# Kernel tuning notes

Measured on AMD Instinct MI355X. Metric: run time of the kernel, lower is better.

The kernel has to match this reference:

```python
import jax, jax.numpy as jnp
import numpy as np

D_MODEL = 1024
NUM_HEADS = 16
HEAD_DIM = D_MODEL // NUM_HEADS
THETA = 10000.0


def setup_inputs() -> dict:
    key = jax.random.key(0)
    k1, k2, k3 = jax.random.split(key, 3)
    B, S = 4, 2048
    x = jax.random.normal(k1, (B, S, D_MODEL), dtype=jnp.float32)
    token_positions = jnp.arange(S, dtype=jnp.int32)
    std_qkv = 2.0 / (D_MODEL + 3 * D_MODEL)
    std_o = 2.0 / (D_MODEL + D_MODEL)
    W_qkv = jax.random.normal(k2, (3 * D_MODEL, D_MODEL), dtype=jnp.float32) * std_qkv
    W_o = jax.random.normal(k3, (D_MODEL, D_MODEL), dtype=jnp.float32) * std_o
    return {"x": x, "token_positions": token_positions, "W_qkv": W_qkv, "W_o": W_o}


def _apply_rope(x, positions):
    # x: [B, H, S, d]; positions: [S]
    d = x.shape[-1]
    inv_freq = 1.0 / THETA ** (2.0 * jnp.arange(0, d // 2, dtype=jnp.float32) / d)
    angle = positions.astype(jnp.float32)[:, None] * inv_freq[None, :]  # [S, d/2]
    cos, sin = jnp.cos(angle), jnp.sin(angle)
    x1, x2 = x[..., 0::2], x[..., 1::2]
    rot = jnp.stack([x1 * cos - x2 * sin, x2 * cos + x1 * sin], axis=-1)
    return rot.reshape(x.shape)


def reference(x, token_positions, W_qkv, W_o):
    B, S, D = x.shape
    H, hd = NUM_HEADS, HEAD_DIM
    qkv = jnp.einsum('bsi,ji->bsj', x, W_qkv)            # [B, S, 3D]
    qkv = qkv.reshape(B, S, 3, H, hd).transpose(2, 0, 3, 1, 4)  # [3, B, H, S, hd]
    q, k, v = qkv[0], qkv[1], qkv[2]
    q = _apply_rope(q, token_positions)
    k = _apply_rope(k, token_positions)
    scores = jnp.einsum('bhqd,bhkd->bhqk', q, k) / jnp.sqrt(jnp.float32(hd))
    causal = jnp.tril(jnp.ones((S, S), dtype=bool))
    scores = jnp.where(causal, scores, -jnp.inf)
    probs = jax.nn.softmax(scores, axis=-1)
    attn = jnp.einsum('bhqk,bhkd->bhqd', probs, v)       # [B, H, S, hd]
    attn = attn.transpose(0, 2, 1, 3).reshape(B, S, D)
    return jnp.einsum('bsi,ji->bsj', attn, W_o)
```

## Files before the change

kernel.cpp:

```cpp
#include <hip/hip_runtime.h>

#define B_ 4
#define S_ 2048
#define D_ 1024
#define H_ 16
#define HD_ 64
#define M_ (B_*S_)
#define NQKV_ (3*D_)

typedef _Float16 f16;
typedef __attribute__((ext_vector_type(4))) _Float16 f16x4;
typedef __attribute__((ext_vector_type(8))) _Float16 f16x8;
typedef __attribute__((ext_vector_type(4))) float f32x4;
typedef __attribute__((ext_vector_type(16))) float f32x16;

__device__ __forceinline__ void gload_lds16(const void* g, void* lds) {
  __builtin_amdgcn_global_load_lds(
      (const __attribute__((address_space(1))) void*)g,
      (__attribute__((address_space(3))) void*)lds, 16, 0, 0);
}

__global__ void cast_kernel(const float* __restrict__ in, f16* __restrict__ out) {
  size_t i = (size_t)(blockIdx.x * 256 + threadIdx.x) * 8;
  float4 a = *reinterpret_cast<const float4*>(in + i);
  float4 b = *reinterpret_cast<const float4*>(in + i + 4);
  f16x8 o;
  o[0] = (f16)a.x; o[1] = (f16)a.y; o[2] = (f16)a.z; o[3] = (f16)a.w;
  o[4] = (f16)b.x; o[5] = (f16)b.y; o[6] = (f16)b.z; o[7] = (f16)b.w;
  *reinterpret_cast<f16x8*>(out + i) = o;
}

__global__ void trig_kernel(const int* __restrict__ pos, float2* __restrict__ tab) {
  int idx = blockIdx.x * 256 + threadIdx.x;
  int s = idx >> 5, t = idx & 31;
  float p = (float)pos[s];
  float invf = exp2f((float)t * -0.4152410118609203f);
  float sn, cs;
  sincosf(p * invf, &sn, &cs);
  tab[idx] = float2{cs, sn};
}

template <int MODE>
__global__ __launch_bounds__(512)
void gemm_bt(const f16* __restrict__ A, const f16* __restrict__ Bt,
             void* __restrict__ Cout, const float2* __restrict__ tab,
             f16* __restrict__ kout, f16* __restrict__ vtout,
             int M, int N, int K) {
  __shared__ __align__(16) f16 As[3][128 * 64];
  __shared__ __align__(16) f16 Bs[3][256 * 64];
  const int tid = threadIdx.x;
  const int w = tid >> 6, l = tid & 63;
  const int nM = M >> 7;
  const int bm = (blockIdx.x % nM) << 7;
  const int bn = (blockIdx.x / nM) << 8;
  const int wrow = (w >> 2) << 6;
  const int wcol = (w & 3) << 6;
  const int lr = l & 15;
  const int lk = (l >> 4) << 3;
  const int orow = (l >> 4) << 2;
  const int swz = (lr & 7) << 3;

  f32x4 acc[4][4];
  #pragma unroll
  for (int i = 0; i < 4; ++i)
    #pragma unroll
    for (int j = 0; j < 4; ++j) acc[i][j] = f32x4{0.f, 0.f, 0.f, 0.f};

  const int sc8 = (tid & 7) * 8;
  const int NT = K >> 6;

  #define STAGE(t_) {                                                         \
    const int buf_ = (t_) % 3, k0_ = (t_) << 6;                               \
    _Pragma("unroll")                                                         \
    for (int i = 0; i < 2; ++i) {                                             \
      int row = (i * 512 + tid) >> 3;                                         \
      gload_lds16(A + (size_t)(bm + row) * K + k0_ + (sc8 ^ ((row & 7) << 3)),\
                  (void*)(&As[buf_][(i * 512 + tid) * 8]));                   \
    }                                                                         \
    _Pragma("unroll")                                                         \
    for (int i = 0; i < 4; ++i) {                                             \
      int row = (i * 512 + tid) >> 3;                                         \
      gload_lds16(Bt + (size_t)(bn + row) * K + k0_ + (sc8 ^ ((row & 7) << 3)),\
                  (void*)(&Bs[buf_][(i * 512 + tid) * 8]));                   \
    }                                                                         \
  }

  STAGE(0);
  STAGE(1);

  for (int t = 0; t < NT; ++t) {
    if (t < NT - 1) {
      asm volatile("s_waitcnt vmcnt(6)" ::: "memory");
    } else {
      asm volatile("s_waitcnt vmcnt(0)" ::: "memory");
    }
    __builtin_amdgcn_sched_barrier(0);
    __builtin_amdgcn_s_barrier();
    __builtin_amdgcn_sched_barrier(0);
    if (t + 2 < NT) STAGE(t + 2);

    const f16* Asc = As[t % 3];
    const f16* Bsc = Bs[t % 3];
    #pragma unroll
    for (int ts = 0; ts < 2; ++ts) {
      f16x8 af[4], bfr[4];
      #pragma unroll
      for (int mi = 0; mi < 4; ++mi)
        af[mi] = *reinterpret_cast<const f16x8*>(
            Asc + (wrow + mi * 16 + lr) * 64 + ((ts * 32 + lk) ^ swz));
      #pragma unroll
      for (int ni = 0; ni < 4; ++ni)
        bfr[ni] = *reinterpret_cast<const f16x8*>(
            Bsc + (wcol + ni * 16 + lr) * 64 + ((ts * 32 + lk) ^ swz));
      #pragma unroll
      for (int mi = 0; mi < 4; ++mi)
        #pragma unroll
        for (int ni = 0; ni < 4; ++ni)
          acc[mi][ni] = __builtin_amdgcn_mfma_f32_16x16x32_f16(bfr[ni], af[mi], acc[mi][ni], 0, 0, 0);
    }
  }
  #undef STAGE

  if (MODE == 0) {
    const int which = bn >> 10;
    const int h = ((bn + wcol) >> 6) & (H_ - 1);
    if (which < 2) {
      f16* dst = which ? kout : (f16*)Cout;
      const float qs = which ? 1.0f : 0.125f * 1.4426950408889634f;
      #pragma unroll
      for (int mi = 0; mi < 4; ++mi) {
        int m = bm + wrow + mi * 16 + lr;
        int b = m >> 11, s = m & (S_ - 1);
        size_t rowbase = ((size_t)(b * H_ + h) * S_ + s) * HD_;
        const float4* trow = reinterpret_cast<const float4*>(tab + (size_t)s * 32);
        #pragma unroll
        for (int ni = 0; ni < 4; ++ni) {
          int d0 = ni * 16 + orow;
          float4 cssn = trow[d0 >> 2];
          float x0 = acc[mi][ni][0], x1 = acc[mi][ni][1];
          float x2 = acc[mi][ni][2], x3 = acc[mi][ni][3];
          f16x4 ov;
          ov[0] = (f16)((x0 * cssn.x - x1 * cssn.y) * qs);
          ov[1] = (f16)((x1 * cssn.x + x0 * cssn.y) * qs);
          ov[2] = (f16)((x2 * cssn.z - x3 * cssn.w) * qs);
          ov[3] = (f16)((x3 * cssn.z + x2 * cssn.w) * qs);
          *reinterpret_cast<f16x4*>(&dst[rowbase + d0]) = ov;
        }
      }
    } else {
      #pragma unroll
      for (int mi = 0; mi < 4; ++mi) {
        int m = bm + wrow + mi * 16 + lr;
        int b = m >> 11, s = m & (S_ - 1);
        size_t base = (size_t)(b * H_ + h) * (HD_ * S_) + s;
        #pragma unroll
        for (int ni = 0; ni < 4; ++ni)
          #pragma unroll
          for (int r = 0; r < 4; ++r)
            vtout[base + (size_t)(ni * 16 + orow + r) * S_] = (f16)acc[mi][ni][r];
      }
    }
  } else {
    float* C = (float*)Cout;
    #pragma unroll
    for (int mi = 0; mi < 4; ++mi) {
      int m = bm + wrow + mi * 16 + lr;
      #pragma unroll
      for (int ni = 0; ni < 4; ++ni) {
        int n = bn + wcol + ni * 16 + orow;
        *reinterpret_cast<float4*>(&C[(size_t)m * N + n]) =
            float4{acc[mi][ni][0], acc[mi][ni][1], acc[mi][ni][2], acc[mi][ni][3]};
      }
    }
  }
}

__global__ __launch_bounds__(256, 4)
void attn_kernel(const f16* __restrict__ q, const f16* __restrict__ k,
                 const f16* __restrict__ vt, f16* __restrict__ attn_out) {
  __shared__ __align__(16) f16 Ks[64 * 64];
  __shared__ __align__(16) f16 Vs[64 * 64];
  __shared__ __align__(16) f16 Ps[4][32 * 64];
  const int tid = threadIdx.x, wq = tid >> 6, l = tid & 63;
  const int lq = l & 31, hi = l >> 5;
  const int bh = blockIdx.x & 63;
  const int qt = 15 - (int)(blockIdx.x >> 6);
  const int q0 = qt << 7;
  const size_t bhoff = (size_t)bh * (S_ * HD_);
  const size_t vtoff = (size_t)bh * (HD_ * S_);
  const int srow = tid >> 3;
  const int sc8 = (tid & 7) * 8;
  const int ssw = sc8 ^ ((srow & 7) << 3);
  const int swz = (lq & 7) << 3;
  const int h = bh & (H_ - 1), b = bh >> 4;
  const int wqmin = q0 + wq * 32;
  const int qrow = wqmin + lq;

  f16x8 qf[4];
  #pragma unroll
  for (int s = 0; s < 4; ++s)
    qf[s] = *reinterpret_cast<const f16x8*>(q + bhoff + (size_t)qrow * HD_ + s * 16 + hi * 8);

  f32x16 o[2];
  float m_run = -1e30f, l_run = 0.f;
  #pragma unroll
  for (int i = 0; i < 2; ++i)
    #pragma unroll
    for (int r = 0; r < 16; ++r) o[i][r] = 0.f;

  f16* Pw = &Ps[wq][0];
  const int ntiles = 2 * qt + 2;
  for (int it = 0; it < ntiles; ++it) {
    const int kv0 = it << 6;
    __syncthreads();
    #pragma unroll
    for (int i = 0; i < 2; ++i) {
      gload_lds16(k + bhoff + (size_t)(kv0 + i * 32 + srow) * HD_ + ssw,
                  (void*)(Ks + (i * 256 + wq * 64) * 8));
      gload_lds16(vt + vtoff + (size_t)(i * 32 + srow) * S_ + kv0 + ssw,
                  (void*)(Vs + (i * 256 + wq * 64) * 8));
    }
    __syncthreads();

    if (kv0 <= wqmin + 31) {
      f32x16 sacc[2];
      #pragma unroll
      for (int kh = 0; kh < 2; ++kh) {
        #pragma unroll
        for (int r = 0; r < 16; ++r) sacc[kh][r] = 0.f;
        #pragma unroll
        for (int s = 0; s < 4; ++s) {
          f16x8 kf = *reinterpret_cast<const f16x8*>(
              Ks + (kh * 32 + lq) * 64 + ((s * 16 + hi * 8) ^ swz));
          sacc[kh] = __builtin_amdgcn_mfma_f32_32x32x16_f16(kf, qf[s], sacc[kh], 0, 0, 0);
        }
      }
      if (kv0 + 63 >= wqmin) {
        #pragma unroll
        for (int kh = 0; kh < 2; ++kh)
          #pragma unroll
          for (int r = 0; r < 16; ++r) {
            int kvg = kv0 + kh * 32 + (r & 3) + 8 * (r >> 2) + 4 * hi;
            if (kvg > qrow) sacc[kh][r] = -1e30f;
          }
      }

      float mloc = -1e30f;
      #pragma unroll
      for (int kh = 0; kh < 2; ++kh)
        #pragma unroll
        for (int r = 0; r < 16; ++r) mloc = fmaxf(mloc, sacc[kh][r]);
      mloc = fmaxf(mloc, __shfl_xor(mloc, 32));
      float mn = fmaxf(m_run, mloc);
      float scale = exp2f(m_run - mn);
      m_run = mn;
      float sloc = 0.f;
      #pragma unroll
      for (int kh = 0; kh < 2; ++kh)
        #pragma unroll
        for (int r = 0; r < 16; ++r) {
          sacc[kh][r] = exp2f(sacc[kh][r] - mn);
          sloc += sacc[kh][r];
        }
      sloc += __shfl_xor(sloc, 32);
      l_run = l_run * scale + sloc;
      #pragma unroll
      for (int i = 0; i < 2; ++i)
        #pragma unroll
        for (int r = 0; r < 16; ++r) o[i][r] *= scale;

      #pragma unroll
      for (int kh = 0; kh < 2; ++kh)
        #pragma unroll
        for (int qd = 0; qd < 4; ++qd) {
          f16x4 pk;
          #pragma unroll
          for (int r = 0; r < 4; ++r) pk[r] = (f16)sacc[kh][qd * 4 + r];
          int kvb = kh * 32 + qd * 8 + hi * 4;
          *reinterpret_cast<f16x4*>(&Pw[lq * 64 + (kvb ^ swz)]) = pk;
        }

      f16x8 pf[4];
      #pragma unroll
      for (int s2 = 0; s2 < 4; ++s2)
        pf[s2] = *reinterpret_cast<const f16x8*>(&Pw[lq * 64 + ((s2 * 16 + hi * 8) ^ swz)]);
      #pragma unroll
      for (int dh = 0; dh < 2; ++dh)
        #pragma unroll
        for (int s2 = 0; s2 < 4; ++s2) {
          f16x8 vf = *reinterpret_cast<const f16x8*>(
              Vs + (dh * 32 + lq) * 64 + ((s2 * 16 + hi * 8) ^ swz));
          o[dh] = __builtin_amdgcn_mfma_f32_32x32x16_f16(vf, pf[s2], o[dh], 0, 0, 0);
        }
    }
  }

  float rl = 1.0f / l_run;
  #pragma unroll
  for (int dh = 0; dh < 2; ++dh)
    #pragma unroll
    for (int qd = 0; qd < 4; ++qd) {
      f16x4 ov;
      #pragma unroll
      for (int r = 0; r < 4; ++r) ov[r] = (f16)(o[dh][qd * 4 + r] * rl);
      int d0 = dh * 32 + qd * 8 + hi * 4;
      *reinterpret_cast<f16x4*>(
          &attn_out[(size_t)(b * S_ + qrow) * D_ + h * HD_ + d0]) = ov;
    }
}

extern "C" void kernel_launch(void* const* d_in, const int* in_sizes, int n_in,
                              void* d_out, int out_size, void* d_ws, size_t ws_size,
                              hipStream_t stream) {
  const float* x    = (const float*)d_in[0];
  const int*   pos  = (const int*)d_in[1];
  const float* wqkv = (const float*)d_in[2];
  const float* wo   = (const float*)d_in[3];
  float* out = (float*)d_out;

  const size_t BHSD = (size_t)B_ * H_ * S_ * HD_;
  f16* xb    = (f16*)d_ws;
  f16* wqkvb = xb + (size_t)M_ * D_;
  f16* wob   = wqkvb + (size_t)NQKV_ * D_;
  f16* qb    = wob + (size_t)D_ * D_;
  f16* kb    = qb + BHSD;
  f16* vtb   = kb + BHSD;
  f16* attnb = vtb + BHSD;
  float2* tab = (float2*)(attnb + BHSD);

  cast_kernel<<<(M_ * D_) / 2048, 256, 0, stream>>>(x, xb);
  cast_kernel<<<(NQKV_ * D_) / 2048, 256, 0, stream>>>(wqkv, wqkvb);
  cast_kernel<<<(D_ * D_) / 2048, 256, 0, stream>>>(wo, wob);
  trig_kernel<<<(S_ * 32) / 256, 256, 0, stream>>>(pos, tab);

  gemm_bt<0><<<(M_ / 128) * (NQKV_ / 256), 512, 0, stream>>>(
      xb, wqkvb, (void*)qb, tab, kb, vtb, M_, NQKV_, D_);

  attn_kernel<<<64 * 16, 256, 0, stream>>>(qb, kb, vtb, attnb);

  gemm_bt<1><<<(M_ / 128) * (D_ / 256), 512, 0, stream>>>(
      attnb, wob, (void*)out, nullptr, nullptr, nullptr, M_, D_, D_);
}
```

Measured before the change: 199.8 us.

## Shrink GEMM tiles to 128x128x32 with double buffering and 256 threads

The projection GEMMs now use 128x128 output tiles, 256-thread blocks (4 waves, each computing 64x64), BK=32 and two LDS buffers in place of the 256-wide, 512-thread, BK=64 triple-buffered version. The LDS swizzle is changed to match, and the prefetch is now issued before the wait, with an extra barrier at the end of each iteration. The goal is smaller LDS use and more resident blocks per CU (launch_bounds 256,4) for better occupancy and latency hiding. In exchange, each block gets less data reuse, there are twice as many K iterations each with two barriers, and only one tile is prefetched ahead.

After: 191.6 us. 1.04x faster.

```diff
diff --git a/kernel.cpp b/kernel.cpp
--- a/kernel.cpp
+++ b/kernel.cpp
@@ -41,24 +41,25 @@
 }
 
 template <int MODE>
-__global__ __launch_bounds__(512)
+__global__ __launch_bounds__(256, 4)
 void gemm_bt(const f16* __restrict__ A, const f16* __restrict__ Bt,
              void* __restrict__ Cout, const float2* __restrict__ tab,
              f16* __restrict__ kout, f16* __restrict__ vtout,
              int M, int N, int K) {
-  __shared__ __align__(16) f16 As[3][128 * 64];
-  __shared__ __align__(16) f16 Bs[3][256 * 64];
+  __shared__ __align__(16) f16 As[2][128 * 32];
+  __shared__ __align__(16) f16 Bs[2][128 * 32];
   const int tid = threadIdx.x;
   const int w = tid >> 6, l = tid & 63;
   const int nM = M >> 7;
-  const int bm = (blockIdx.x % nM) << 7;
-  const int bn = (blockIdx.x / nM) << 8;
-  const int wrow = (w >> 2) << 6;
-  const int wcol = (w & 3) << 6;
+  const int bm = (int)(blockIdx.x % nM) << 7;
+  const int bn = (int)(blockIdx.x / nM) << 7;
+  const int wrow = (w >> 1) << 6;
+  const int wcol = (w & 1) << 6;
   const int lr = l & 15;
   const int lk = (l >> 4) << 3;
   const int orow = (l >> 4) << 2;
-  const int swz = (lr & 7) << 3;
+  const int swzr = (lr & 3) << 3;
+  const int NT = K >> 5;
 
   f32x4 acc[4][4];
   #pragma unroll
@@ -66,60 +67,56 @@
     #pragma unroll
     for (int j = 0; j < 4; ++j) acc[i][j] = f32x4{0.f, 0.f, 0.f, 0.f};
 
-  const int sc8 = (tid & 7) * 8;
-  const int NT = K >> 6;
-
-  #define STAGE(t_) {                                                         \
-    const int buf_ = (t_) % 3, k0_ = (t_) << 6;                               \
-    _Pragma("unroll")                                                         \
-    for (int i = 0; i < 2; ++i) {                                             \
-      int row = (i * 512 + tid) >> 3;                                         \
-      gload_lds16(A + (size_t)(bm + row) * K + k0_ + (sc8 ^ ((row & 7) << 3)),\
-                  (void*)(&As[buf_][(i * 512 + tid) * 8]));                   \
-    }                                                                         \
-    _Pragma("unroll")                                                         \
-    for (int i = 0; i < 4; ++i) {                                             \
-      int row = (i * 512 + tid) >> 3;                                         \
-      gload_lds16(Bt + (size_t)(bn + row) * K + k0_ + (sc8 ^ ((row & 7) << 3)),\
-                  (void*)(&Bs[buf_][(i * 512 + tid) * 8]));                   \
-    }                                                                         \
-  }
+  const int srow4 = tid >> 2;
+  const int ssw = ((tid & 3) * 8) ^ ((srow4 & 3) << 3);
+
+#define STAGE(t_) do {                                                    \
+    const int buf_ = (t_) & 1; const int k0_ = (t_) << 5;                 \
+    _Pragma("unroll")                                                     \
+    for (int p = 0; p < 2; ++p)                                           \
+      gload_lds16(A + (size_t)(bm + p * 64 + srow4) * K + k0_ + ssw,      \
+                  (void*)(&As[buf_][(p * 256 + tid) * 8]));               \
+    _Pragma("unroll")                                                     \
+    for (int p = 0; p < 2; ++p)                                           \
+      gload_lds16(Bt + (size_t)(bn + p * 64 + srow4) * K + k0_ + ssw,     \
+                  (void*)(&Bs[buf_][(p * 256 + tid) * 8]));               \
+  } while (0)
 
   STAGE(0);
-  STAGE(1);
 
   for (int t = 0; t < NT; ++t) {
-    if (t < NT - 1) {
-      asm volatile("s_waitcnt vmcnt(6)" ::: "memory");
+    if (t + 1 < NT) {
+      STAGE(t + 1);
+      asm volatile("s_waitcnt vmcnt(4)" ::: "memory");
     } else {
       asm volatile("s_waitcnt vmcnt(0)" ::: "memory");
     }
     __builtin_amdgcn_sched_barrier(0);
     __builtin_amdgcn_s_barrier();
     __builtin_amdgcn_sched_barrier(0);
-    if (t + 2 < NT) STAGE(t + 2);
-
-    const f16* Asc = As[t % 3];
-    const f16* Bsc = Bs[t % 3];
-    #pragma unroll
-    for (int ts = 0; ts < 2; ++ts) {
-      f16x8 af[4], bfr[4];
-      #pragma unroll
-      for (int mi = 0; mi < 4; ++mi)
-        af[mi] = *reinterpret_cast<const f16x8*>(
-            Asc + (wrow + mi * 16 + lr) * 64 + ((ts * 32 + lk) ^ swz));
+
+    const f16* Asc = As[t & 1];
+    const f16* Bsc = Bs[t & 1];
+    f16x8 af[4], bf[4];
+    #pragma unroll
+    for (int mi = 0; mi < 4; ++mi)
+      af[mi] = *reinterpret_cast<const f16x8*>(
+          Asc + (wrow + mi * 16 + lr) * 32 + (lk ^ swzr));
+    #pragma unroll
+    for (int ni = 0; ni < 4; ++ni)
+      bf[ni] = *reinterpret_cast<const f16x8*>(
+          Bsc + (wcol + ni * 16 + lr) * 32 + (lk ^ swzr));
+    #pragma unroll
+    for (int mi = 0; mi < 4; ++mi)
       #pragma unroll
       for (int ni = 0; ni < 4; ++ni)
-        bfr[ni] = *reinterpret_cast<const f16x8*>(
-            Bsc + (wcol + ni * 16 + lr) * 64 + ((ts * 32 + lk) ^ swz));
-      #pragma unroll
-      for (int mi = 0; mi < 4; ++mi)
-        #pragma unroll
-        for (int ni = 0; ni < 4; ++ni)
-          acc[mi][ni] = __builtin_amdgcn_mfma_f32_16x16x32_f16(bfr[ni], af[mi], acc[mi][ni], 0, 0, 0);
-    }
+        acc[mi][ni] = __builtin_amdgcn_mfma_f32_16x16x32_f16(bf[ni], af[mi], acc[mi][ni], 0, 0, 0);
+
+    __builtin_amdgcn_sched_barrier(0);
+    __builtin_amdgcn_s_barrier();
+    __builtin_amdgcn_sched_barrier(0);
   }
-  #undef STAGE
+#undef STAGE
 
   if (MODE == 0) {
     const int which = bn >> 10;
@@ -333,11 +330,11 @@
   cast_kernel<<<(D_ * D_) / 2048, 256, 0, stream>>>(wo, wob);
   trig_kernel<<<(S_ * 32) / 256, 256, 0, stream>>>(pos, tab);
 
-  gemm_bt<0><<<(M_ / 128) * (NQKV_ / 256), 512, 0, stream>>>(
+  gemm_bt<0><<<(M_ / 128) * (NQKV_ / 128), 256, 0, stream>>>(
       xb, wqkvb, (void*)qb, tab, kb, vtb, M_, NQKV_, D_);
 
   attn_kernel<<<64 * 16, 256, 0, stream>>>(qb, kb, vtb, attnb);
 
-  gemm_bt<1><<<(M_ / 128) * (D_ / 256), 512, 0, stream>>>(
+  gemm_bt<1><<<(M_ / 128) * (D_ / 128), 256, 0, stream>>>(
       attnb, wob, (void*)out, nullptr, nullptr, nullptr, M_, D_, D_);
 }
```
